# Performance work log

Hardware: AMD Instinct MI355X
Metric: run time of the kernel (lower is better)

Reference implementation:

```python
import jax, jax.numpy as jnp
import numpy as np

HIDDEN = 1152
NUM_HEADS = 16
HEAD_DIM = HIDDEN // NUM_HEADS  # 72
SEQ = 4096


def rotate_half(x):
    x1 = x[..., : x.shape[-1] // 2]
    x2 = x[..., x.shape[-1] // 2 :]
    return jnp.concatenate((-x2, x1), axis=-1)


def setup_inputs() -> dict:
    key = jax.random.key(0)
    ks = jax.random.split(key, 8)
    hidden_states = jax.random.normal(ks[0], (SEQ, HIDDEN), dtype=jnp.float32)
    cu_seqlens = jnp.sort(jax.random.randint(ks[1], (3,), 0, SEQ)).astype(jnp.int32)
    # rotary embeddings: realistic cos/sin tables
    pos = jnp.arange(SEQ, dtype=jnp.float32)[:, None]
    inv_freq = 1.0 / (10000.0 ** (jnp.arange(0, HEAD_DIM, 2, dtype=jnp.float32) / HEAD_DIM))
    freqs = pos * inv_freq[None, :]  # (SEQ, HEAD_DIM//2)
    emb = jnp.concatenate([freqs, freqs], axis=-1)  # (SEQ, HEAD_DIM)
    cos = jnp.cos(emb)
    sin = jnp.sin(emb)
    std = 0.02
    Wqkv = jax.random.normal(ks[2], (HIDDEN, 3 * HIDDEN), dtype=jnp.float32) * std
    bqkv = jnp.zeros((3 * HIDDEN,), dtype=jnp.float32)
    Wproj = jax.random.normal(ks[3], (HIDDEN, HIDDEN), dtype=jnp.float32) * std
    bproj = jnp.zeros((HIDDEN,), dtype=jnp.float32)
    return {
        "hidden_states": hidden_states,
        "cu_seqlens": cu_seqlens,
        "cos": cos,
        "sin": sin,
        "Wqkv": Wqkv,
        "bqkv": bqkv,
        "Wproj": Wproj,
        "bproj": bproj,
    }


def reference(hidden_states, cu_seqlens, cos, sin, Wqkv, bqkv, Wproj, bproj):
    seq_len = hidden_states.shape[0]
    scale = HEAD_DIM ** -0.5
    qkv = hidden_states @ Wqkv + bqkv  # (S, 3*H)
    qkv = qkv.reshape(seq_len, 3, NUM_HEADS, HEAD_DIM).transpose(1, 0, 2, 3)
    q, k, v = qkv[0], qkv[1], qkv[2]  # each (S, nH, hd)
    # inline RoPE in fp32
    orig_dtype = q.dtype
    qf = q.astype(jnp.float32)
    kf = k.astype(jnp.float32)
    c = cos[:, None, :].astype(jnp.float32)
    s = sin[:, None, :].astype(jnp.float32)
    q = (qf * c + rotate_half(qf) * s).astype(orig_dtype)
    k = (kf * c + rotate_half(kf) * s).astype(orig_dtype)
    # (nH, S, hd)
    q = q.transpose(1, 0, 2)
    k = k.transpose(1, 0, 2)
    v = v.transpose(1, 0, 2)
    attn = jnp.einsum('hqd,hkd->hqk', q, k) * scale
    attn = jax.nn.softmax(attn, axis=-1)
    out = jnp.einsum('hqk,hkd->hqd', attn, v)  # (nH, S, hd)
    out = out.transpose(1, 0, 2).reshape(seq_len, HIDDEN)
    return out @ Wproj + bproj
```

## Files before the change

kernel.cpp:

```cpp
#include <hip/hip_runtime.h>
#include <hip/hip_bf16.h>
#include <stdint.h>

#define SEQ 4096
#define HID 1152
#define NH  16
#define HD  72
#define N3  3456
#define DQ  80
#define QBLK 256
#define TILE_ELEMS 14336

typedef __bf16 bf16;
typedef __bf16 bf16x8 __attribute__((ext_vector_type(8)));
typedef float  f32x4  __attribute__((ext_vector_type(4)));
typedef float  f32x16 __attribute__((ext_vector_type(16)));
typedef uint32_t u32x4 __attribute__((ext_vector_type(4)));

#define EXP2F(x) __builtin_amdgcn_exp2f(x)
#define PLSWAP(a, b) asm("v_permlane32_swap_b32 %0, %1" : "+v"(a), "+v"(b))

__device__ __forceinline__ void gload_lds16(const void* g, void* l) {
    __builtin_amdgcn_global_load_lds(
        (__attribute__((address_space(1))) void*)(void*)g,
        (__attribute__((address_space(3))) void*)l, 16, 0, 0);
}
__device__ __forceinline__ uint16_t bfbits(float x) {
    return __builtin_bit_cast(uint16_t, (bf16)x);
}

__device__ __forceinline__ int xcd_swz(int orig, int nwg) {
    return (orig & 7) * (nwg >> 3) + (orig >> 3);
}

__global__ __launch_bounds__(256)
void prep(const float* __restrict__ hidden, const float* __restrict__ Wqkv,
          const float* __restrict__ Wproj, bf16* __restrict__ hid_b,
          bf16* __restrict__ WqkvT, bf16* __restrict__ WprojT)
{
    __shared__ float tl[32][33];
    int b = blockIdx.x, tid = threadIdx.x;
    if (b < 2304) {
        int i = b * 256 + tid;
        const float4* p = (const float4*)hidden + (size_t)i * 2;
        float4 a = p[0], c = p[1];
        bf16x8 o;
        o[0]=(bf16)a.x; o[1]=(bf16)a.y; o[2]=(bf16)a.z; o[3]=(bf16)a.w;
        o[4]=(bf16)c.x; o[5]=(bf16)c.y; o[6]=(bf16)c.z; o[7]=(bf16)c.w;
        ((bf16x8*)hid_b)[i] = o;
        return;
    }
    const float* in; bf16* out; int R, C, c0, r0;
    if (b < 6192) {
        int bb = b - 2304;
        in = Wqkv; out = WqkvT; R = HID; C = N3;
        c0 = (bb % 108) * 32; r0 = (bb / 108) * 32;
    } else {
        int bb = b - 6192;
        in = Wproj; out = WprojT; R = HID; C = HID;
        c0 = (bb % 36) * 32; r0 = (bb / 36) * 32;
    }
    int tx = tid & 31, ty = tid >> 5;
#pragma unroll
    for (int i = 0; i < 4; ++i)
        tl[ty + 8*i][tx] = in[(size_t)(r0 + ty + 8*i) * C + c0 + tx];
    __syncthreads();
#pragma unroll
    for (int i = 0; i < 4; ++i)
        out[(size_t)(c0 + ty + 8*i) * R + r0 + tx] = (bf16)tl[tx][ty + 8*i];
}

template<int OUT_F32>
__global__ __launch_bounds__(256)
void gemm_bt(const bf16* __restrict__ A, const bf16* __restrict__ BT,
             const float* __restrict__ bias, void* __restrict__ out,
             int M, int N, int K)
{
    __shared__ __align__(16) bf16 As[128 * 32];
    __shared__ __align__(16) bf16 Bs[128 * 32];
    int tid = threadIdx.x;
    int lane = tid & 63, w = tid >> 6;
    int wm = w & 1, wn = w >> 1;
    int nwg  = gridDim.x * gridDim.y;
    int wgid = xcd_swz(blockIdx.y * gridDim.x + blockIdx.x, nwg);
    int m0 = (wgid % gridDim.x) * 128, n0 = (wgid / gridDim.x) * 128;
    int lq = lane & 15, lk = lane >> 4;

    f32x4 acc[4][4] = {};

    for (int k0 = 0; k0 < K; k0 += 32) {
        __syncthreads();
#pragma unroll
        for (int i = 0; i < 2; ++i) {
            int c = w * 128 + i * 64 + lane;
            const bf16* ga = A  + (size_t)(m0 + (c >> 2)) * K + k0 + (c & 3) * 8;
            const bf16* gb = BT + (size_t)(n0 + (c >> 2)) * K + k0 + (c & 3) * 8;
            gload_lds16(ga, (char*)As + (w * 128 + i * 64) * 16);
            gload_lds16(gb, (char*)Bs + (w * 128 + i * 64) * 16);
        }
        __syncthreads();
        bf16x8 af[4], bfr[4];
#pragma unroll
        for (int m = 0; m < 4; ++m)
            af[m] = *(const bf16x8*)&As[(wm * 64 + m * 16 + lq) * 32 + lk * 8];
#pragma unroll
        for (int n = 0; n < 4; ++n)
            bfr[n] = *(const bf16x8*)&Bs[(wn * 64 + n * 16 + lq) * 32 + lk * 8];
#pragma unroll
        for (int m = 0; m < 4; ++m)
#pragma unroll
            for (int n = 0; n < 4; ++n)
                acc[m][n] = __builtin_amdgcn_mfma_f32_16x16x32_bf16(af[m], bfr[n], acc[m][n], 0, 0, 0);
    }

    int rb = m0 + wm * 64, cb = n0 + wn * 64;
#pragma unroll
    for (int m = 0; m < 4; ++m) {
#pragma unroll
        for (int n = 0; n < 4; ++n) {
            int col = cb + n * 16 + lq;
            float b = bias[col];
#pragma unroll
            for (int r = 0; r < 4; ++r) {
                int row = rb + m * 16 + lk * 4 + r;
                float v = acc[m][n][r] + b;
                if (OUT_F32) ((float*)out)[(size_t)row * N + col] = v;
                else         ((bf16*)out)[(size_t)row * N + col] = (bf16)v;
            }
        }
    }
}

__global__ __launch_bounds__(256)
void pack(const bf16* __restrict__ qkv, const float* __restrict__ cs,
          const float* __restrict__ sn, bf16* __restrict__ Qp,
          bf16* __restrict__ KVp)
{
    __shared__ __align__(16) bf16 tl[64][80];
    int b = blockIdx.x, tid = threadIdx.x;
    if (b < 32768) {
        int idx = b * 256 + tid;
        int dd = idx & 127;
        int s  = (idx >> 7) & (SEQ - 1);
        int h  = idx >> 19;
        float qv = 0.f, kv = 0.f;
        if (dd < HD) {
            const bf16* row = qkv + (size_t)s * N3 + h * HD;
            float c  = cs[s * HD + dd], si = sn[s * HD + dd];
            int   dp = (dd < 36) ? dd + 36 : dd - 36;
            float sg = (dd < 36) ? -1.f : 1.f;
            float qa = (float)row[dd],       qb = (float)row[dp];
            float ka = (float)row[HID + dd], kb = (float)row[HID + dp];
            qv = (qa * c + sg * qb * si) * (0.11785113019775793f * 1.4426950408889634f);
            kv =  ka * c + sg * kb * si;
        }
        int t = s >> 6, key = s & 63;
        int chunk = key * 16 + ((dd >> 3) ^ (key & 15));
        KVp[((size_t)(h * 64 + t)) * TILE_ELEMS + chunk * 8 + (dd & 7)] = (bf16)kv;
        if (dd < DQ) Qp[((size_t)h * SEQ + s) * DQ + dd] = (bf16)qv;
        return;
    }
    int bb = b - 32768;
    int t = bb & 63, h = bb >> 6, s0 = t * 64;
    for (int i = tid; i < 64 * 9; i += 256) {
        int key = i / 9, c8 = (i % 9) * 8;
        *(bf16x8*)&tl[key][c8] =
            *(const bf16x8*)&qkv[(size_t)(s0 + key) * N3 + 2 * HID + h * HD + c8];
    }
    __syncthreads();
    bf16* dst = KVp + ((size_t)(h * 64 + t)) * TILE_ELEMS + 8192;
    for (int vcid = tid; vcid < 768; vcid += 256) {
        int d = vcid >> 3, cpos = vcid & 7;
        int kb8 = (cpos ^ (d & 7)) << 3;
        bf16x8 v;
#pragma unroll
        for (int j = 0; j < 8; ++j)
            v[j] = (d < HD) ? tl[kb8 + j][d] : ((d == HD) ? (bf16)1.f : (bf16)0.f);
        *(bf16x8*)&dst[vcid * 8] = v;
    }
}

__global__ __launch_bounds__(512, 2)
void attn_fwd11(const bf16* __restrict__ Qp, const bf16* __restrict__ KVp,
                bf16* __restrict__ Oout)
{
    __shared__ __align__(16) char smem[86016];

    const int wgid = xcd_swz(blockIdx.x, gridDim.x);
    const int h  = wgid >> 4;
    const int q0 = (wgid & 15) * QBLK;
    const int tid = threadIdx.x, lane = tid & 63, w = tid >> 6;
    const int ql = lane & 31, hi = lane >> 5;
    const int q  = q0 + w * 32 + ql;

    bf16x8 qf[5];
    const bf16* qbase = Qp + ((size_t)h * SEQ + q) * DQ + hi * 8;
#pragma unroll
    for (int ks = 0; ks < 5; ++ks) qf[ks] = *(const bf16x8*)(qbase + ks * 16);

    int aK[5], aV[4];
#pragma unroll
    for (int ks = 0; ks < 5; ++ks)
        aK[ks] = ql * 256 + (((ks * 2 + hi) ^ (ql & 15)) * 16);
#pragma unroll
    for (int u = 0; u < 4; ++u)
        aV[u] = 16384 + ql * 128 + (((u * 2 + hi) ^ (ql & 7)) * 16);

    f32x16 o[3] = {};

    const bf16* kvbase = KVp + (size_t)h * (64 * TILE_ELEMS) + (size_t)tid * 8;

#define STAGE(T, DB) do {                                                      \
        const bf16* s_ = kvbase + (size_t)(T) * TILE_ELEMS;                    \
        char* d_ = smem + (DB) + tid * 16;                                     \
        _Pragma("unroll")                                                      \
        for (int j_ = 0; j_ < 3; ++j_)                                         \
            gload_lds16(s_ + j_ * 4096, d_ + j_ * 8192);                       \
        if (tid < 256) gload_lds16(s_ + 12288, d_ + 24576);                    \
    } while (0)

    auto qk = [&](const char* bK, f32x16& sa, f32x16& sb) {
        __builtin_amdgcn_s_setprio(1);
#pragma unroll
        for (int ks = 0; ks < 5; ++ks) {
            bf16x8 kf = *(const bf16x8*)(bK + aK[ks]);
            sa = __builtin_amdgcn_mfma_f32_32x32x16_bf16(kf, qf[ks], sa, 0, 0, 0);
        }
#pragma unroll
        for (int ks = 0; ks < 5; ++ks) {
            bf16x8 kf = *(const bf16x8*)(bK + 8192 + aK[ks]);
            sb = __builtin_amdgcn_mfma_f32_32x32x16_bf16(kf, qf[ks], sb, 0, 0, 0);
        }
        __builtin_amdgcn_s_setprio(0);
    };

    auto expv = [&](const f32x16& sa, const f32x16& sb, const char* bV) {
        uint32_t wd[16];
#pragma unroll
        for (int i = 0; i < 8; ++i) {
            wd[i]   = (uint32_t)bfbits(EXP2F(sa[2*i])) | ((uint32_t)bfbits(EXP2F(sa[2*i+1])) << 16);
            wd[8+i] = (uint32_t)bfbits(EXP2F(sb[2*i])) | ((uint32_t)bfbits(EXP2F(sb[2*i+1])) << 16);
        }
        PLSWAP(wd[0], wd[2]);   PLSWAP(wd[1], wd[3]);
        PLSWAP(wd[4], wd[6]);   PLSWAP(wd[5], wd[7]);
        PLSWAP(wd[8], wd[10]);  PLSWAP(wd[9], wd[11]);
        PLSWAP(wd[12], wd[14]); PLSWAP(wd[13], wd[15]);
        u32x4 u0 = {wd[0],wd[1],wd[2],wd[3]},   u1 = {wd[4],wd[5],wd[6],wd[7]};
        u32x4 u2 = {wd[8],wd[9],wd[10],wd[11]}, u3 = {wd[12],wd[13],wd[14],wd[15]};
        bf16x8 pb[4] = { __builtin_bit_cast(bf16x8, u0), __builtin_bit_cast(bf16x8, u1),
                         __builtin_bit_cast(bf16x8, u2), __builtin_bit_cast(bf16x8, u3) };
        __builtin_amdgcn_s_setprio(1);
#pragma unroll
        for (int db = 0; db < 3; ++db)
#pragma unroll
            for (int u = 0; u < 4; ++u) {
                bf16x8 vf = *(const bf16x8*)(bV + db * 4096 + aV[u]);
                o[db] = __builtin_amdgcn_mfma_f32_32x32x16_bf16(vf, pb[u], o[db], 0, 0, 0);
            }
        __builtin_amdgcn_s_setprio(0);
    };

    f32x16 pa = {}, pb_ = {};

    STAGE(0, 0);
    asm volatile("s_waitcnt vmcnt(0)" ::: "memory");
    __builtin_amdgcn_s_barrier();
    STAGE(1, 28672);
    qk(smem, pa, pb_);
    asm volatile("s_waitcnt vmcnt(0)" ::: "memory");
    __builtin_amdgcn_s_barrier();

#define BODY(T, KB, VB, SB) do {                                               \
        if ((T) < 63) STAGE((T) + 1, SB);                                      \
        f32x16 ca = {}, cb = {};                                               \
        qk(smem + (KB), ca, cb);                                               \
        expv(pa, pb_, smem + (VB));                                            \
        pa = ca; pb_ = cb;                                                     \
        __builtin_amdgcn_sched_barrier(0);                                     \
        asm volatile("s_waitcnt vmcnt(0)" ::: "memory");                       \
        __builtin_amdgcn_s_barrier();                                          \
    } while (0)

    for (int t = 1; t < 64; t += 3) {
        BODY(t,     28672, 0,     57344);
        BODY(t + 1, 57344, 28672, 0);
        BODY(t + 2, 0,     57344, 28672);
    }
    expv(pa, pb_, smem);
#undef BODY
#undef STAGE

    __syncthreads();
    bf16* Os = (bf16*)smem;
    {
        float lv  = o[2][4];
        float lo_ = __shfl_xor(lv, 32);
        float invl = 1.0f / (hi ? lo_ : lv);
        int qloc = w * 32 + ql;
#pragma unroll
        for (int db = 0; db < 3; ++db)
#pragma unroll
            for (int r = 0; r < 16; ++r) {
                int dloc = (r & 3) + 8 * (r >> 2) + 4 * hi;
                int d = db * 32 + dloc;
                if (d < HD) Os[qloc * 82 + d] = (bf16)(o[db][r] * invl);
            }
    }
    __syncthreads();
    for (int i = tid; i < QBLK * 36; i += 512) {
        int row = i / 36, c = i % 36;
        uint32_t val = *(const uint32_t*)((const char*)Os + row * 164 + c * 4);
        *(uint32_t*)((char*)Oout + (size_t)(q0 + row) * 2304 + h * 144 + c * 4) = val;
    }
}

extern "C" void kernel_launch(void* const* d_in, const int* in_sizes, int n_in,
                              void* d_out, int out_size, void* d_ws, size_t ws_size,
                              hipStream_t stream)
{
    const float* hidden = (const float*)d_in[0];
    const float* cosT  = (const float*)d_in[2];
    const float* sinT  = (const float*)d_in[3];
    const float* Wqkv  = (const float*)d_in[4];
    const float* bqkv  = (const float*)d_in[5];
    const float* Wproj = (const float*)d_in[6];
    const float* bproj = (const float*)d_in[7];

    char* ws = (char*)d_ws;
    size_t off = 0;
    auto alloc = [&](size_t bytes) {
        char* p = ws + off;
        off += (bytes + 255) & ~(size_t)255;
        return p;
    };
    bf16* hid_b  = (bf16*)alloc((size_t)SEQ * HID * 2);
    bf16* WqkvT  = (bf16*)alloc((size_t)N3  * HID * 2);
    bf16* WprojT = (bf16*)alloc((size_t)HID * HID * 2);
    bf16* qkv_b  = (bf16*)alloc((size_t)SEQ * N3  * 2);
    bf16* Qp     = (bf16*)alloc((size_t)NH * SEQ * DQ * 2);
    bf16* KVp    = (bf16*)alloc((size_t)NH * 64 * TILE_ELEMS * 2);
    bf16* attno  = hid_b;

    prep<<<7488, 256, 0, stream>>>(hidden, Wqkv, Wproj, hid_b, WqkvT, WprojT);
    gemm_bt<0><<<dim3(SEQ / 128, N3 / 128), 256, 0, stream>>>(hid_b, WqkvT, bqkv, qkv_b,
                                                              SEQ, N3, HID);
    pack<<<33792, 256, 0, stream>>>(qkv_b, cosT, sinT, Qp, KVp);
    attn_fwd11<<<dim3(SEQ / QBLK * NH), 512, 0, stream>>>(Qp, KVp, attno);
    gemm_bt<1><<<dim3(SEQ / 128, HID / 128), 256, 0, stream>>>(attno, WprojT, bproj, d_out,
                                                               SEQ, HID, HID);
}
```

Before: 221.5 us.

## Double GEMM K-tile to 64 with XOR-swizzled LDS and remap attention blocks per XCD

```diff
diff --git a/kernel.cpp b/kernel.cpp
--- a/kernel.cpp
+++ b/kernel.cpp
@@ -76,8 +76,8 @@
              const float* __restrict__ bias, void* __restrict__ out,
              int M, int N, int K)
 {
-    __shared__ __align__(16) bf16 As[128 * 32];
-    __shared__ __align__(16) bf16 Bs[128 * 32];
+    __shared__ __align__(16) bf16 As[128 * 64];
+    __shared__ __align__(16) bf16 Bs[128 * 64];
     int tid = threadIdx.x;
     int lane = tid & 63, w = tid >> 6;
     int wm = w & 1, wn = w >> 1;
@@ -86,31 +86,38 @@
     int m0 = (wgid % gridDim.x) * 128, n0 = (wgid / gridDim.x) * 128;
     int lq = lane & 15, lk = lane >> 4;
 
+    int kx0 = ((lk ^ (lq & 7)) << 4);
+    int kx1 = (((4 + lk) ^ (lq & 7)) << 4);
+
     f32x4 acc[4][4] = {};
 
-    for (int k0 = 0; k0 < K; k0 += 32) {
+    for (int k0 = 0; k0 < K; k0 += 64) {
         __syncthreads();
 #pragma unroll
-        for (int i = 0; i < 2; ++i) {
-            int c = w * 128 + i * 64 + lane;
-            const bf16* ga = A  + (size_t)(m0 + (c >> 2)) * K + k0 + (c & 3) * 8;
-            const bf16* gb = BT + (size_t)(n0 + (c >> 2)) * K + k0 + (c & 3) * 8;
-            gload_lds16(ga, (char*)As + (w * 128 + i * 64) * 16);
-            gload_lds16(gb, (char*)Bs + (w * 128 + i * 64) * 16);
+        for (int j = 0; j < 4; ++j) {
+            int c = j * 256 + tid;
+            int row = c >> 3, kc = c & 7;
+            int koff = k0 + ((kc ^ (row & 7)) << 3);
+            gload_lds16(A  + (size_t)(m0 + row) * K + koff, (char*)As + c * 16);
+            gload_lds16(BT + (size_t)(n0 + row) * K + koff, (char*)Bs + c * 16);
         }
         __syncthreads();
-        bf16x8 af[4], bfr[4];
-#pragma unroll
-        for (int m = 0; m < 4; ++m)
-            af[m] = *(const bf16x8*)&As[(wm * 64 + m * 16 + lq) * 32 + lk * 8];
-#pragma unroll
-        for (int n = 0; n < 4; ++n)
-            bfr[n] = *(const bf16x8*)&Bs[(wn * 64 + n * 16 + lq) * 32 + lk * 8];
-#pragma unroll
-        for (int m = 0; m < 4; ++m)
+#pragma unroll
+        for (int ks = 0; ks < 2; ++ks) {
+            int kx = ks ? kx1 : kx0;
+            bf16x8 af[4], bfr[4];
+#pragma unroll
+            for (int m = 0; m < 4; ++m)
+                af[m] = *(const bf16x8*)((char*)As + (wm * 64 + m * 16 + lq) * 128 + kx);
 #pragma unroll
             for (int n = 0; n < 4; ++n)
-                acc[m][n] = __builtin_amdgcn_mfma_f32_16x16x32_bf16(af[m], bfr[n], acc[m][n], 0, 0, 0);
+                bfr[n] = *(const bf16x8*)((char*)Bs + (wn * 64 + n * 16 + lq) * 128 + kx);
+#pragma unroll
+            for (int m = 0; m < 4; ++m)
+#pragma unroll
+                for (int n = 0; n < 4; ++n)
+                    acc[m][n] = __builtin_amdgcn_mfma_f32_16x16x32_bf16(af[m], bfr[n], acc[m][n], 0, 0, 0);
+        }
     }
 
     int rb = m0 + wm * 64, cb = n0 + wn * 64;
@@ -186,9 +193,10 @@
 {
     __shared__ __align__(16) char smem[86016];
 
-    const int wgid = xcd_swz(blockIdx.x, gridDim.x);
-    const int h  = wgid >> 4;
-    const int q0 = (wgid & 15) * QBLK;
+    const int o = blockIdx.x;
+    const int x = o & 7, s = o >> 3;
+    const int h  = x * 2 + (s >> 4);
+    const int q0 = (s & 15) * QBLK;
     const int tid = threadIdx.x, lane = tid & 63, w = tid >> 6;
     const int ql = lane & 31, hi = lane >> 5;
     const int q  = q0 + w * 32 + ql;
@@ -206,7 +214,7 @@
     for (int u = 0; u < 4; ++u)
         aV[u] = 16384 + ql * 128 + (((u * 2 + hi) ^ (ql & 7)) * 16);
 
-    f32x16 o[3] = {};
+    f32x16 o_[3] = {};
 
     const bf16* kvbase = KVp + (size_t)h * (64 * TILE_ELEMS) + (size_t)tid * 8;
 
@@ -255,7 +263,7 @@
 #pragma unroll
             for (int u = 0; u < 4; ++u) {
                 bf16x8 vf = *(const bf16x8*)(bV + db * 4096 + aV[u]);
-                o[db] = __builtin_amdgcn_mfma_f32_32x32x16_bf16(vf, pb[u], o[db], 0, 0, 0);
+                o_[db] = __builtin_amdgcn_mfma_f32_32x32x16_bf16(vf, pb[u], o_[db], 0, 0, 0);
             }
         __builtin_amdgcn_s_setprio(0);
     };
@@ -293,7 +301,7 @@
     __syncthreads();
     bf16* Os = (bf16*)smem;
     {
-        float lv  = o[2][4];
+        float lv  = o_[2][4];
         float lo_ = __shfl_xor(lv, 32);
         float invl = 1.0f / (hi ? lo_ : lv);
         int qloc = w * 32 + ql;
@@ -303,7 +311,7 @@
             for (int r = 0; r < 16; ++r) {
                 int dloc = (r & 3) + 8 * (r >> 2) + 4 * hi;
                 int d = db * 32 + dloc;
-                if (d < HD) Os[qloc * 82 + d] = (bf16)(o[db][r] * invl);
+                if (d < HD) Os[qloc * 82 + d] = (bf16)(o_[db][r] * invl);
             }
     }
     __syncthreads();
```

Result: faster. 205.1 us (-7.4%).
